# Optimization experiments

Hardware: AMD Instinct MI355X
Metric: run time of the kernel (lower is better)

Reference implementation:

```python
import jax, jax.numpy as jnp
import numpy as np

B, S, H, I = 2, 2048, 4096, 11008  # batch, seq, hidden_size, intermediate_size (Llama-7B)


def setup_inputs() -> dict:
    key = jax.random.key(0)
    ks = jax.random.split(key, 11)
    # int8 activations and weights (SmoothQuant W8A8)
    hidden_states = jax.random.randint(ks[0], (B, S, H), -128, 128, dtype=jnp.int8)
    w_gate = jax.random.randint(ks[1], (I, H), -128, 128, dtype=jnp.int8)
    w_up = jax.random.randint(ks[2], (I, H), -128, 128, dtype=jnp.int8)
    w_down = jax.random.randint(ks[3], (H, I), -128, 128, dtype=jnp.int8)
    # dequant scales (alpha = input_scale * weight_scale), small positive
    gate_a = jax.random.uniform(ks[4], (1,), dtype=jnp.float32) * 1e-4 + 1e-5
    up_a = jax.random.uniform(ks[5], (1,), dtype=jnp.float32) * 1e-4 + 1e-5
    down_a = jax.random.uniform(ks[6], (1,), dtype=jnp.float32) * 1e-4 + 1e-5
    # fp32 biases
    gate_b = jax.random.normal(ks[7], (I,), dtype=jnp.float32) * 0.01
    up_b = jax.random.normal(ks[8], (I,), dtype=jnp.float32) * 0.01
    down_b = jax.random.normal(ks[9], (H,), dtype=jnp.float32) * 0.01
    # requantization scale for down_proj input
    down_scale = jax.random.uniform(ks[10], (1,), dtype=jnp.float32) * 0.05 + 0.01
    return {
        "hidden_states": hidden_states,
        "w_gate": w_gate, "w_up": w_up, "w_down": w_down,
        "gate_a": gate_a, "gate_b": gate_b,
        "up_a": up_a, "up_b": up_b,
        "down_a": down_a, "down_b": down_b,
        "down_scale": down_scale,
    }


def _i8_gemm(x_i8, w_i8):
    return jnp.einsum("bsk,nk->bsn", x_i8, w_i8, preferred_element_type=jnp.int32)


def reference(hidden_states, w_gate, w_up, w_down,
              gate_a, gate_b, up_a, up_b, down_a, down_b, down_scale):
    # gate_proj: W8A8 GEMM -> dequant (alpha) + fp32 bias -> fused SiLU
    g = _i8_gemm(hidden_states, w_gate).astype(jnp.float32) * gate_a[0] + gate_b
    gate_out = g * jax.nn.sigmoid(g)  # SiLU
    # up_proj: W8A8 GEMM -> dequant + fp32 bias
    up_out = _i8_gemm(hidden_states, w_up).astype(jnp.float32) * up_a[0] + up_b
    inter = gate_out * up_out
    # requantize to int8 for down_proj input
    q = jnp.clip(jnp.round(inter / down_scale[0]), -128, 127).astype(jnp.int8)
    # down_proj: W8A8 GEMM -> dequant + fp32 bias
    down_out = _i8_gemm(q, w_down).astype(jnp.float32) * down_a[0] + down_b
    return down_out  # [B, S, H] fp32
```

## Files before the change

### kernel.cpp

```cpp
#include <hip/hip_runtime.h>
#include <cstdint>


typedef int v4i  __attribute__((ext_vector_type(4)));
typedef int v16i __attribute__((ext_vector_type(16)));

typedef const void __attribute__((address_space(1)))* gas_ptr;
typedef void __attribute__((address_space(3)))* las_ptr;

static constexpr int M_TOT = 4096;
static constexpr int HDIM  = 4096;
static constexpr int IDIM  = 11008;

#define BM 128
#define BN 128
#define BK 128

__global__ __launch_bounds__(256) void k_pack(const int* __restrict__ src,
                                              int8_t* __restrict__ dst, int n16) {
  int t = blockIdx.x * blockDim.x + threadIdx.x;
  if (t >= n16) return;
  const int4* s = (const int4*)(src) + t * 4;
  int4 v0 = s[0], v1 = s[1], v2 = s[2], v3 = s[3];
  int p0 = (v0.x & 0xff) | ((v0.y & 0xff) << 8) | ((v0.z & 0xff) << 16) | (v0.w << 24);
  int p1 = (v1.x & 0xff) | ((v1.y & 0xff) << 8) | ((v1.z & 0xff) << 16) | (v1.w << 24);
  int p2 = (v2.x & 0xff) | ((v2.y & 0xff) << 8) | ((v2.z & 0xff) << 16) | (v2.w << 24);
  int p3 = (v3.x & 0xff) | ((v3.y & 0xff) << 8) | ((v3.z & 0xff) << 16) | (v3.w << 24);
  ((int4*)dst)[t] = make_int4(p0, p1, p2, p3);
}

__device__ __forceinline__ void async_stage_16kb(const int8_t* __restrict__ gbase,
                                                 int ld, int8_t* lds, int tid) {
#pragma unroll
  for (int it = 0; it < 4; ++it) {
    const int chunk = it * 256 + tid;
    const int row   = chunk >> 3;
    const int slot  = chunk & 7;
    const int gch   = slot ^ (row & 7);
    const int8_t* g = gbase + row * ld + gch * 16;
    int8_t* l = lds + chunk * 16;
    __builtin_amdgcn_global_load_lds((gas_ptr)g, (las_ptr)l, 16, 0, 0);
  }
}

__device__ __forceinline__ v4i frag_ld(const int8_t* lds, int row, int kc, int half) {
  const int ch  = kc + half;
  const int sch = ch ^ (row & 7);
  return *(const v4i*)(lds + row * 128 + sch * 16);
}

#define MFMA_I8(a, b, c) __builtin_amdgcn_mfma_i32_32x32x32_i8((a), (b), (c), 0, 0, 0)

__global__ __launch_bounds__(256, 2) void k_gateup(
    const int8_t* __restrict__ X,
    const int8_t* __restrict__ Wg,
    const int8_t* __restrict__ Wu,
    const float* __restrict__ gate_a, const float* __restrict__ gate_b,
    const float* __restrict__ up_a,   const float* __restrict__ up_b,
    const float* __restrict__ down_scale,
    int8_t* __restrict__ Q) {
  __shared__ __align__(16) int8_t sA[BM * BK];
  __shared__ __align__(16) int8_t sG[BN * BK];
  __shared__ __align__(16) int8_t sU[BN * BK];

  const int tid  = threadIdx.x;
  const int lane = tid & 63;
  const int wave = tid >> 6;
  const int wm   = wave >> 1;
  const int wn   = wave & 1;
  const int half = lane >> 5;
  const int ln31 = lane & 31;

  const int m0 = blockIdx.x * BM;
  const int n0 = blockIdx.y * BN;

  const int8_t* Ab = X  + (size_t)m0 * HDIM;
  const int8_t* Gb = Wg + (size_t)n0 * HDIM;
  const int8_t* Ub = Wu + (size_t)n0 * HDIM;

  v16i accG[2][2], accU[2][2];
#pragma unroll
  for (int i = 0; i < 2; ++i)
#pragma unroll
    for (int j = 0; j < 2; ++j)
#pragma unroll
      for (int e = 0; e < 16; ++e) { accG[i][j][e] = 0; accU[i][j][e] = 0; }

  const int rA = wm * 64 + ln31;
  const int rB = wn * 64 + ln31;

  for (int k0 = 0; k0 < HDIM; k0 += BK) {
    async_stage_16kb(Ab + k0, HDIM, sA, tid);
    async_stage_16kb(Gb + k0, HDIM, sG, tid);
    async_stage_16kb(Ub + k0, HDIM, sU, tid);
    __syncthreads();
#pragma unroll
    for (int kc = 0; kc < 8; kc += 2) {
      v4i a0 = frag_ld(sA, rA,      kc, half);
      v4i a1 = frag_ld(sA, rA + 32, kc, half);
      v4i g0 = frag_ld(sG, rB,      kc, half);
      v4i g1 = frag_ld(sG, rB + 32, kc, half);
      v4i u0 = frag_ld(sU, rB,      kc, half);
      v4i u1 = frag_ld(sU, rB + 32, kc, half);
      accG[0][0] = MFMA_I8(a0, g0, accG[0][0]);
      accG[0][1] = MFMA_I8(a0, g1, accG[0][1]);
      accG[1][0] = MFMA_I8(a1, g0, accG[1][0]);
      accG[1][1] = MFMA_I8(a1, g1, accG[1][1]);
      accU[0][0] = MFMA_I8(a0, u0, accU[0][0]);
      accU[0][1] = MFMA_I8(a0, u1, accU[0][1]);
      accU[1][0] = MFMA_I8(a1, u0, accU[1][0]);
      accU[1][1] = MFMA_I8(a1, u1, accU[1][1]);
    }
    __syncthreads();
  }

  const float ga = gate_a[0];
  const float ua = up_a[0];
  const float inv_ds = 1.0f / down_scale[0];

#pragma unroll
  for (int tm = 0; tm < 2; ++tm) {
#pragma unroll
    for (int tn = 0; tn < 2; ++tn) {
      const int n = n0 + wn * 64 + tn * 32 + ln31;
      const float gb = gate_b[n];
      const float ub = up_b[n];
#pragma unroll
      for (int r = 0; r < 16; ++r) {
        const int row_l = (r & 3) + 8 * (r >> 2) + 4 * half;
        const int m = m0 + wm * 64 + tm * 32 + row_l;
        const float g = (float)accG[tm][tn][r] * ga + gb;
        const float u = (float)accU[tm][tn][r] * ua + ub;
        const float sg = g / (1.0f + __expf(-g));
        const float inter = sg * u;
        float qf = rintf(inter * inv_ds);
        qf = fminf(127.0f, fmaxf(-128.0f, qf));
        Q[(size_t)m * IDIM + n] = (int8_t)qf;
      }
    }
  }
}

__global__ __launch_bounds__(256, 2) void k_down(
    const int8_t* __restrict__ Q,
    const int8_t* __restrict__ Wd,
    const float* __restrict__ down_a, const float* __restrict__ down_b,
    float* __restrict__ Out) {
  __shared__ __align__(16) int8_t sA[BM * BK];
  __shared__ __align__(16) int8_t sB[BN * BK];

  const int tid  = threadIdx.x;
  const int lane = tid & 63;
  const int wave = tid >> 6;
  const int wm   = wave >> 1;
  const int wn   = wave & 1;
  const int half = lane >> 5;
  const int ln31 = lane & 31;

  const int m0 = blockIdx.x * BM;
  const int n0 = blockIdx.y * BN;

  const int8_t* Ab = Q  + (size_t)m0 * IDIM;
  const int8_t* Bb = Wd + (size_t)n0 * IDIM;

  v16i acc[2][2];
#pragma unroll
  for (int i = 0; i < 2; ++i)
#pragma unroll
    for (int j = 0; j < 2; ++j)
#pragma unroll
      for (int e = 0; e < 16; ++e) acc[i][j][e] = 0;

  const int rA = wm * 64 + ln31;
  const int rB = wn * 64 + ln31;

  for (int k0 = 0; k0 < IDIM; k0 += BK) {
    async_stage_16kb(Ab + k0, IDIM, sA, tid);
    async_stage_16kb(Bb + k0, IDIM, sB, tid);
    __syncthreads();
#pragma unroll
    for (int kc = 0; kc < 8; kc += 2) {
      v4i a0 = frag_ld(sA, rA,      kc, half);
      v4i a1 = frag_ld(sA, rA + 32, kc, half);
      v4i b0 = frag_ld(sB, rB,      kc, half);
      v4i b1 = frag_ld(sB, rB + 32, kc, half);
      acc[0][0] = MFMA_I8(a0, b0, acc[0][0]);
      acc[0][1] = MFMA_I8(a0, b1, acc[0][1]);
      acc[1][0] = MFMA_I8(a1, b0, acc[1][0]);
      acc[1][1] = MFMA_I8(a1, b1, acc[1][1]);
    }
    __syncthreads();
  }

  const float da = down_a[0];
#pragma unroll
  for (int tm = 0; tm < 2; ++tm) {
#pragma unroll
    for (int tn = 0; tn < 2; ++tn) {
      const int n = n0 + wn * 64 + tn * 32 + ln31;
      const float db = down_b[n];
#pragma unroll
      for (int r = 0; r < 16; ++r) {
        const int row_l = (r & 3) + 8 * (r >> 2) + 4 * half;
        const int m = m0 + wm * 64 + tm * 32 + row_l;
        Out[(size_t)m * HDIM + n] = (float)acc[tm][tn][r] * da + db;
      }
    }
  }
}

extern "C" void kernel_launch(void* const* d_in, const int* in_sizes, int n_in,
                              void* d_out, int out_size, void* d_ws, size_t ws_size,
                              hipStream_t stream) {
  const int* X32        = (const int*)d_in[0];
  const int* Wg32       = (const int*)d_in[1];
  const int* Wu32       = (const int*)d_in[2];
  const int* Wd32       = (const int*)d_in[3];
  const float* gate_a   = (const float*)d_in[4];
  const float* gate_b   = (const float*)d_in[5];
  const float* up_a     = (const float*)d_in[6];
  const float* up_b     = (const float*)d_in[7];
  const float* down_a   = (const float*)d_in[8];
  const float* down_b   = (const float*)d_in[9];
  const float* down_scale = (const float*)d_in[10];
  float* Out = (float*)d_out;

  const size_t nX = (size_t)M_TOT * HDIM;
  const size_t nW = (size_t)IDIM * HDIM;

  int8_t* Q   = (int8_t*)d_ws;
  int8_t* Xp  = Q   + nW;
  int8_t* Wgp = Xp  + nX;
  int8_t* Wup = Wgp + nW;
  int8_t* Wdp = Wup + nW;

  {
    int n16 = (int)(nX / 16);
    k_pack<<<(n16 + 255) / 256, 256, 0, stream>>>(X32, Xp, n16);
    n16 = (int)(nW / 16);
    k_pack<<<(n16 + 255) / 256, 256, 0, stream>>>(Wg32, Wgp, n16);
    k_pack<<<(n16 + 255) / 256, 256, 0, stream>>>(Wu32, Wup, n16);
    k_pack<<<(n16 + 255) / 256, 256, 0, stream>>>(Wd32, Wdp, n16);
  }

  dim3 g1(M_TOT / BM, IDIM / BN);
  k_gateup<<<g1, dim3(256), 0, stream>>>(Xp, Wgp, Wup, gate_a, gate_b, up_a, up_b,
                                         down_scale, Q);
  dim3 g2(M_TOT / BM, HDIM / BN);
  k_down<<<g2, dim3(256), 0, stream>>>(Q, Wdp, down_a, down_b, Out);
}
```

Baseline: 1.131 ms.

## Enlarge down-proj tile to 256x128 and fuse int8 pack launches

The down-projection GEMM now uses 256x128 block tiles, with each wave computing a 128x64 sub-tile, which doubles A-fragment reuse of B and halves the number of blocks. The four separate int32-to-int8 pack launches are merged into a single kernel that dispatches by index range. Larger tiles raise register and LDS use per block, and with fewer blocks occupancy and tail balance may drop.

```diff
diff --git a/kernel.cpp b/kernel.cpp
--- a/kernel.cpp
+++ b/kernel.cpp
@@ -16,10 +16,8 @@
 #define BN 128
 #define BK 128
 
-__global__ __launch_bounds__(256) void k_pack(const int* __restrict__ src,
-                                              int8_t* __restrict__ dst, int n16) {
-  int t = blockIdx.x * blockDim.x + threadIdx.x;
-  if (t >= n16) return;
+__device__ __forceinline__ void pack16(const int* __restrict__ src,
+                                       int8_t* __restrict__ dst, int t) {
   const int4* s = (const int4*)(src) + t * 4;
   int4 v0 = s[0], v1 = s[1], v2 = s[2], v3 = s[3];
   int p0 = (v0.x & 0xff) | ((v0.y & 0xff) << 8) | ((v0.z & 0xff) << 16) | (v0.w << 24);
@@ -27,6 +25,26 @@
   int p2 = (v2.x & 0xff) | ((v2.y & 0xff) << 8) | ((v2.z & 0xff) << 16) | (v2.w << 24);
   int p3 = (v3.x & 0xff) | ((v3.y & 0xff) << 8) | ((v3.z & 0xff) << 16) | (v3.w << 24);
   ((int4*)dst)[t] = make_int4(p0, p1, p2, p3);
+}
+
+static constexpr int CX = (M_TOT * HDIM) / 16;
+static constexpr int CW = (IDIM * HDIM) / 16;
+static constexpr int CTOT = CX + 3 * CW;
+
+__global__ __launch_bounds__(256) void k_pack_all(
+    const int* __restrict__ X32, const int* __restrict__ Wg32,
+    const int* __restrict__ Wu32, const int* __restrict__ Wd32,
+    int8_t* __restrict__ Xp, int8_t* __restrict__ Wgp,
+    int8_t* __restrict__ Wup, int8_t* __restrict__ Wdp) {
+  int t = blockIdx.x * blockDim.x + threadIdx.x;
+  if (t >= CTOT) return;
+  if (t < CX)               { pack16(X32,  Xp,  t); return; }
+  t -= CX;
+  if (t < CW)               { pack16(Wg32, Wgp, t); return; }
+  t -= CW;
+  if (t < CW)               { pack16(Wu32, Wup, t); return; }
+  t -= CW;
+  pack16(Wd32, Wdp, t);
 }
 
 __device__ __forceinline__ void async_stage_16kb(const int8_t* __restrict__ gbase,
@@ -146,8 +164,8 @@
     const int8_t* __restrict__ Wd,
     const float* __restrict__ down_a, const float* __restrict__ down_b,
     float* __restrict__ Out) {
-  __shared__ __align__(16) int8_t sA[BM * BK];
-  __shared__ __align__(16) int8_t sB[BN * BK];
+  __shared__ __align__(16) int8_t sA[256 * BK];
+  __shared__ __align__(16) int8_t sB[128 * BK];
 
   const int tid  = threadIdx.x;
   const int lane = tid & 63;
@@ -157,44 +175,51 @@
   const int half = lane >> 5;
   const int ln31 = lane & 31;
 
-  const int m0 = blockIdx.x * BM;
-  const int n0 = blockIdx.y * BN;
+  const int m0 = blockIdx.x * 256;
+  const int n0 = blockIdx.y * 128;
 
   const int8_t* Ab = Q  + (size_t)m0 * IDIM;
   const int8_t* Bb = Wd + (size_t)n0 * IDIM;
 
-  v16i acc[2][2];
-#pragma unroll
-  for (int i = 0; i < 2; ++i)
+  v16i acc[4][2];
+#pragma unroll
+  for (int i = 0; i < 4; ++i)
 #pragma unroll
     for (int j = 0; j < 2; ++j)
 #pragma unroll
       for (int e = 0; e < 16; ++e) acc[i][j][e] = 0;
 
-  const int rA = wm * 64 + ln31;
+  const int rA = wm * 128 + ln31;
   const int rB = wn * 64 + ln31;
 
   for (int k0 = 0; k0 < IDIM; k0 += BK) {
     async_stage_16kb(Ab + k0, IDIM, sA, tid);
+    async_stage_16kb(Ab + (size_t)128 * IDIM + k0, IDIM, sA + 128 * BK, tid);
     async_stage_16kb(Bb + k0, IDIM, sB, tid);
     __syncthreads();
 #pragma unroll
     for (int kc = 0; kc < 8; kc += 2) {
       v4i a0 = frag_ld(sA, rA,      kc, half);
       v4i a1 = frag_ld(sA, rA + 32, kc, half);
+      v4i a2 = frag_ld(sA, rA + 64, kc, half);
+      v4i a3 = frag_ld(sA, rA + 96, kc, half);
       v4i b0 = frag_ld(sB, rB,      kc, half);
       v4i b1 = frag_ld(sB, rB + 32, kc, half);
       acc[0][0] = MFMA_I8(a0, b0, acc[0][0]);
       acc[0][1] = MFMA_I8(a0, b1, acc[0][1]);
       acc[1][0] = MFMA_I8(a1, b0, acc[1][0]);
       acc[1][1] = MFMA_I8(a1, b1, acc[1][1]);
+      acc[2][0] = MFMA_I8(a2, b0, acc[2][0]);
+      acc[2][1] = MFMA_I8(a2, b1, acc[2][1]);
+      acc[3][0] = MFMA_I8(a3, b0, acc[3][0]);
+      acc[3][1] = MFMA_I8(a3, b1, acc[3][1]);
     }
     __syncthreads();
   }
 
   const float da = down_a[0];
 #pragma unroll
-  for (int tm = 0; tm < 2; ++tm) {
+  for (int tm = 0; tm < 4; ++tm) {
 #pragma unroll
     for (int tn = 0; tn < 2; ++tn) {
       const int n = n0 + wn * 64 + tn * 32 + ln31;
@@ -202,7 +227,7 @@
 #pragma unroll
       for (int r = 0; r < 16; ++r) {
         const int row_l = (r & 3) + 8 * (r >> 2) + 4 * half;
-        const int m = m0 + wm * 64 + tm * 32 + row_l;
+        const int m = m0 + wm * 128 + tm * 32 + row_l;
         Out[(size_t)m * HDIM + n] = (float)acc[tm][tn][r] * da + db;
       }
     }
@@ -234,18 +259,12 @@
   int8_t* Wup = Wgp + nW;
   int8_t* Wdp = Wup + nW;
 
-  {
-    int n16 = (int)(nX / 16);
-    k_pack<<<(n16 + 255) / 256, 256, 0, stream>>>(X32, Xp, n16);
-    n16 = (int)(nW / 16);
-    k_pack<<<(n16 + 255) / 256, 256, 0, stream>>>(Wg32, Wgp, n16);
-    k_pack<<<(n16 + 255) / 256, 256, 0, stream>>>(Wu32, Wup, n16);
-    k_pack<<<(n16 + 255) / 256, 256, 0, stream>>>(Wd32, Wdp, n16);
-  }
+  k_pack_all<<<(CTOT + 255) / 256, 256, 0, stream>>>(X32, Wg32, Wu32, Wd32,
+                                                     Xp, Wgp, Wup, Wdp);
 
   dim3 g1(M_TOT / BM, IDIM / BN);
   k_gateup<<<g1, dim3(256), 0, stream>>>(Xp, Wgp, Wup, gate_a, gate_b, up_a, up_b,
                                          down_scale, Q);
-  dim3 g2(M_TOT / BM, HDIM / BN);
+  dim3 g2(M_TOT / 256, HDIM / 128);
   k_down<<<g2, dim3(256), 0, stream>>>(Q, Wdp, down_a, down_b, Out);
 }
```

New measurement: 1.123 ms. Within noise of the previous version (-0.7%).
